# Performance work log

Hardware: AMD Instinct MI355X
Metric: run time of the kernel (lower is better)

## Reference

```python
import jax, jax.numpy as jnp
import numpy as np

FRAC_BITS = 16            # fixed-point fractional bits (MPC fixedpoint precision)
SCALE = float(1 << FRAC_BITS)

def fxp(v):
    """Emulate dup_with_precision: round value to the fixed-point grid with
    FRAC_BITS fractional bits. Straight-through (identity) gradient, matching
    the MPC backward pass which propagates gradients through truncation."""
    return v + jax.lax.stop_gradient(jnp.round(v * SCALE) / SCALE - v)


def setup_inputs() -> dict:
    key = jax.random.key(0)
    kx, kw = jax.random.split(key)
    in_dim, out_dim, batch = 4096, 4096, 2048
    x = jax.random.normal(kx, (batch, in_dim), dtype=jnp.float32)
    # Dense_Local init: w ~ N(0, 1/sqrt(in_dim+1)), b = zeros
    w = jax.random.normal(kw, (in_dim, out_dim), dtype=jnp.float32) / np.sqrt(in_dim + 1)
    b = jnp.zeros((out_dim,), dtype=jnp.float32)
    return {"x": x, "w": w, "b": b}


def reference(x, w, b):
    # quantize operands to the fixed-point grid (values live on the grid in MPC)
    xq = fxp(x)
    wq = fxp(w)
    # y = x @ w, then dup_with_precision(x.fixedpoint): truncate product back
    y = fxp(jnp.matmul(xq, wq))           # [batch, out_dim]
    # + bias
    y = y + fxp(b)
    # secure ReLU: s = drelu_local(y) (sign bit), y = relu(y, s) = y * s
    s = y >= 0
    y = jnp.where(s, y, jnp.zeros((), dtype=y.dtype))
    # final dup_with_precision(new_fixedpoint=x.fixedpoint)
    return fxp(y)
```

## Files before the change

kernel.cpp:

```cpp
#include <hip/hip_runtime.h>
#include <hip/hip_bf16.h>
#include <stdint.h>

#define M_DIM 2048
#define N_DIM 4096
#define K_DIM 4096

#define NT 64

typedef short short8 __attribute__((ext_vector_type(8)));
typedef float f32x4 __attribute__((ext_vector_type(4)));

typedef __attribute__((address_space(1))) unsigned int gu32;
typedef __attribute__((address_space(3))) unsigned int lu32;

__device__ static inline unsigned short f32_to_bf16(float f) {
  union { float f; unsigned int u; } v; v.f = f;
  unsigned int u = v.u;
  u += 0x7FFFu + ((u >> 16) & 1u);
  return (unsigned short)(u >> 16);
}

__global__ void cvt_x_kernel(const float* __restrict__ in, unsigned short* __restrict__ out) {
  size_t i = ((size_t)blockIdx.x * blockDim.x + threadIdx.x) * 8;
  f32x4 a = *(const f32x4*)(in + i);
  f32x4 b = *(const f32x4*)(in + i + 4);
  short8 o;
  o[0] = (short)f32_to_bf16(a[0]); o[1] = (short)f32_to_bf16(a[1]);
  o[2] = (short)f32_to_bf16(a[2]); o[3] = (short)f32_to_bf16(a[3]);
  o[4] = (short)f32_to_bf16(b[0]); o[5] = (short)f32_to_bf16(b[1]);
  o[6] = (short)f32_to_bf16(b[2]); o[7] = (short)f32_to_bf16(b[3]);
  *(short8*)(out + i) = o;
}

__global__ void transpose_cvt_w_kernel(const float* __restrict__ w, unsigned short* __restrict__ wt) {
  __shared__ unsigned short tile[64][64 + 8];
  int bn = blockIdx.x * 64;
  int bk = blockIdx.y * 64;
  int t = threadIdx.x;
  int c4 = (t & 15) * 4;
  int r0 = t >> 4;
#pragma unroll
  for (int p = 0; p < 4; ++p) {
    int r = r0 + p * 16;
    f32x4 v = *(const f32x4*)(w + (size_t)(bk + r) * N_DIM + bn + c4);
    tile[c4 + 0][r] = f32_to_bf16(v[0]);
    tile[c4 + 1][r] = f32_to_bf16(v[1]);
    tile[c4 + 2][r] = f32_to_bf16(v[2]);
    tile[c4 + 3][r] = f32_to_bf16(v[3]);
  }
  __syncthreads();
  int orow = t >> 2;
  int oc = (t & 3) * 16;
  short8 lo, hi;
#pragma unroll
  for (int j = 0; j < 8; ++j) {
    lo[j] = (short)tile[orow][oc + j];
    hi[j] = (short)tile[orow][oc + 8 + j];
  }
  unsigned short* op = wt + (size_t)(bn + orow) * K_DIM + bk + oc;
  *(short8*)(op) = lo;
  *(short8*)(op + 8) = hi;
}


__global__ __launch_bounds__(512) void gemm8_kernel(
    const unsigned short* __restrict__ A, const unsigned short* __restrict__ Bt,
    const float* __restrict__ bias, float* __restrict__ C) {
  __shared__ unsigned short sm16[3 * 24576];
  char* smem = (char*)&sm16[0];

  const int tid = threadIdx.x;
  const int lane = tid & 63;
  const int w = tid >> 6;
  const int wm = w >> 2, wn = w & 3;

  const int id = blockIdx.x;
  const int x = id & 7, j = id >> 3;
  const int by = ((x >> 2) << 3) + (j >> 2);
  const int bx = ((x & 3) << 2) + (j & 3);
  const int r0 = by * 128, c0 = bx * 256;

  const int l8 = lane >> 3, l7 = lane & 7;
  const int chunkE = ((l7 ^ (l8 & 7)) << 3);
  const unsigned short* Ag = A + (size_t)(r0 + w * 16 + l8) * K_DIM + chunkE;
  const unsigned short* Bg = Bt + (size_t)(c0 + w * 32 + l8) * K_DIM + chunkE;
  const int aL0 = w * 2048;
  const int bL0 = 16384 + w * 4096;

#define GL(gp, ldsoff) __builtin_amdgcn_global_load_lds((gu32*)(gp), (lu32*)(smem + (ldsoff)), 16, 0, 0)
#define STAGE_P0(t, sb)                                       \
  do {                                                        \
    GL(Ag + (size_t)(t) * 64, (sb) + aL0);                    \
    GL(Ag + (size_t)(t) * 64 + 8 * (size_t)K_DIM, (sb) + aL0 + 1024); \
    GL(Bg + (size_t)(t) * 64, (sb) + bL0);                    \
  } while (0)
#define STAGE_P1(t, sb)                                       \
  do {                                                        \
    GL(Bg + (size_t)(t) * 64 + 8 * (size_t)K_DIM, (sb) + bL0 + 1024);  \
    GL(Bg + (size_t)(t) * 64 + 16 * (size_t)K_DIM, (sb) + bL0 + 2048); \
    GL(Bg + (size_t)(t) * 64 + 24 * (size_t)K_DIM, (sb) + bL0 + 3072); \
  } while (0)

  const int l15 = lane & 15, hi = lane >> 4;
  const int aR = (wm * 64 + l15) * 64;
  const int bR = 8192 + (wn * 64 + l15) * 64;
  const int slot0 = ((hi ^ l7) << 3);
  const int slot1 = (((4 + hi) ^ l7) << 3);

  f32x4 acc[4][4] = {};

  STAGE_P0(0, 0); STAGE_P1(0, 0);
  STAGE_P0(1, 49152); STAGE_P1(1, 49152);

  int cs = 0;
  for (int t = 0; t < NT; ++t) {
    const int sE = cs * 24576;
    const int stB = (cs == 0 ? 2 : cs - 1) * 49152;
    const bool doStage = (t + 2) < NT;

    if (t < NT - 1) asm volatile("s_waitcnt vmcnt(6)" ::: "memory");
    else            asm volatile("s_waitcnt vmcnt(0)" ::: "memory");
    asm volatile("s_barrier" ::: "memory");

    {
      short8 a[4], b[4];
#pragma unroll
      for (int m = 0; m < 4; ++m) a[m] = *(const short8*)(sm16 + sE + aR + m * 1024 + slot0);
#pragma unroll
      for (int n = 0; n < 4; ++n) b[n] = *(const short8*)(sm16 + sE + bR + n * 1024 + slot0);
      if (doStage) STAGE_P0(t + 2, stB);
      asm volatile("s_barrier" ::: "memory");
      __builtin_amdgcn_s_setprio(1);
#pragma unroll
      for (int m = 0; m < 4; ++m)
#pragma unroll
        for (int n = 0; n < 4; ++n)
          acc[m][n] = __builtin_amdgcn_mfma_f32_16x16x32_bf16(a[m], b[n], acc[m][n], 0, 0, 0);
      __builtin_amdgcn_s_setprio(0);
      asm volatile("s_barrier" ::: "memory");
    }
    {
      short8 a[4], b[4];
#pragma unroll
      for (int m = 0; m < 4; ++m) a[m] = *(const short8*)(sm16 + sE + aR + m * 1024 + slot1);
#pragma unroll
      for (int n = 0; n < 4; ++n) b[n] = *(const short8*)(sm16 + sE + bR + n * 1024 + slot1);
      if (doStage) STAGE_P1(t + 2, stB);
      asm volatile("s_barrier" ::: "memory");
      __builtin_amdgcn_s_setprio(1);
#pragma unroll
      for (int m = 0; m < 4; ++m)
#pragma unroll
        for (int n = 0; n < 4; ++n)
          acc[m][n] = __builtin_amdgcn_mfma_f32_16x16x32_bf16(a[m], b[n], acc[m][n], 0, 0, 0);
      __builtin_amdgcn_s_setprio(0);
      asm volatile("s_barrier" ::: "memory");
    }
    cs = (cs == 2) ? 0 : cs + 1;
  }

  const float S = 65536.0f, IS = 1.0f / 65536.0f;
  const int lr = hi * 4;
#pragma unroll
  for (int n = 0; n < 4; ++n) {
    int gcol = c0 + wn * 64 + n * 16 + l15;
    float bq = rintf(bias[gcol] * S) * IS;
#pragma unroll
    for (int m = 0; m < 4; ++m) {
      int grow = r0 + wm * 64 + m * 16 + lr;
      float* outp = C + (size_t)grow * N_DIM + gcol;
#pragma unroll
      for (int r = 0; r < 4; ++r) {
        float t = rintf(acc[m][n][r] * S) * IS + bq;
        t = t > 0.0f ? t : 0.0f;
        outp[(size_t)r * N_DIM] = t;
      }
    }
  }
#undef GL
#undef STAGE_P0
#undef STAGE_P1
}

__global__ __launch_bounds__(256, 2) void gemm_fb_kernel(
    const float* __restrict__ Xf, const float* __restrict__ Wf,
    const float* __restrict__ bias, float* __restrict__ C) {
  __shared__ unsigned short As[128][64];
  __shared__ unsigned short Bs[128][64];
  int tid = threadIdx.x;
  int lane = tid & 63;
  int wid = tid >> 6;
  int wr = wid >> 1, wc = wid & 1;
  int r0 = blockIdx.y * 128;
  int c0 = blockIdx.x * 128;
  f32x4 acc[4][4] = {};
  for (int kt = 0; kt < K_DIM / 64; ++kt) {
    __syncthreads();
    int ar = tid >> 1;
    int ac = (tid & 1) * 32;
    const float* xp = Xf + (size_t)(r0 + ar) * K_DIM + kt * 64 + ac;
#pragma unroll
    for (int jj = 0; jj < 8; ++jj) {
      f32x4 v = *(const f32x4*)(xp + jj * 4);
      As[ar][ac + jj * 4 + 0] = f32_to_bf16(v[0]);
      As[ar][ac + jj * 4 + 1] = f32_to_bf16(v[1]);
      As[ar][ac + jj * 4 + 2] = f32_to_bf16(v[2]);
      As[ar][ac + jj * 4 + 3] = f32_to_bf16(v[3]);
    }
    int bk_ = tid >> 2;
    int bc = (tid & 3) * 32;
    const float* wp = Wf + (size_t)(kt * 64 + bk_) * N_DIM + c0 + bc;
#pragma unroll
    for (int jj = 0; jj < 8; ++jj) {
      f32x4 v = *(const f32x4*)(wp + jj * 4);
      Bs[bc + jj * 4 + 0][bk_] = f32_to_bf16(v[0]);
      Bs[bc + jj * 4 + 1][bk_] = f32_to_bf16(v[1]);
      Bs[bc + jj * 4 + 2][bk_] = f32_to_bf16(v[2]);
      Bs[bc + jj * 4 + 3][bk_] = f32_to_bf16(v[3]);
    }
    __syncthreads();
#pragma unroll
    for (int ks = 0; ks < 2; ++ks) {
      int co = ks * 32 + (lane >> 4) * 8;
      int rA = wr * 64 + (lane & 15);
      int rB = wc * 64 + (lane & 15);
      short8 a[4], b[4];
#pragma unroll
      for (int m = 0; m < 4; ++m) a[m] = *(const short8*)&As[rA + m * 16][co];
#pragma unroll
      for (int n = 0; n < 4; ++n) b[n] = *(const short8*)&Bs[rB + n * 16][co];
#pragma unroll
      for (int m = 0; m < 4; ++m)
#pragma unroll
        for (int n = 0; n < 4; ++n)
          acc[m][n] = __builtin_amdgcn_mfma_f32_16x16x32_bf16(a[m], b[n], acc[m][n], 0, 0, 0);
    }
  }
  const float S = 65536.0f, IS = 1.0f / 65536.0f;
  int lr = (lane >> 4) * 4;
  int lc = lane & 15;
#pragma unroll
  for (int n = 0; n < 4; ++n) {
    int gcol = c0 + wc * 64 + n * 16 + lc;
    float bq = rintf(bias[gcol] * S) * IS;
#pragma unroll
    for (int m = 0; m < 4; ++m) {
      int grow = r0 + wr * 64 + m * 16 + lr;
      float* outp = C + (size_t)grow * N_DIM + gcol;
#pragma unroll
      for (int r = 0; r < 4; ++r) {
        float t = rintf(acc[m][n][r] * S) * IS + bq;
        t = t > 0.0f ? t : 0.0f;
        outp[(size_t)r * N_DIM] = t;
      }
    }
  }
}

extern "C" void kernel_launch(void* const* d_in, const int* in_sizes, int n_in,
                              void* d_out, int out_size, void* d_ws, size_t ws_size,
                              hipStream_t stream) {
  const float* x = (const float*)d_in[0];
  const float* w = (const float*)d_in[1];
  const float* b = (const float*)d_in[2];
  float* out = (float*)d_out;

  size_t needA = (size_t)M_DIM * K_DIM * sizeof(unsigned short);
  size_t needB = (size_t)K_DIM * N_DIM * sizeof(unsigned short);

  if (ws_size >= needA + needB) {
    unsigned short* Abf = (unsigned short*)d_ws;
    unsigned short* Btbf = (unsigned short*)((char*)d_ws + needA);
    cvt_x_kernel<<<(M_DIM * (size_t)K_DIM / 8 + 255) / 256, 256, 0, stream>>>(x, Abf);
    transpose_cvt_w_kernel<<<dim3(N_DIM / 64, K_DIM / 64), 256, 0, stream>>>(w, Btbf);
    gemm8_kernel<<<256, 512, 0, stream>>>(Abf, Btbf, b, out);
  } else {
    gemm_fb_kernel<<<dim3(N_DIM / 128, M_DIM / 128), 256, 0, stream>>>(x, w, b, out);
  }
}
```

Measured before the change: 94.33 us.

## Merge half-iteration phases into one per-tile step with a single barrier

```diff
diff --git a/kernel.cpp b/kernel.cpp
--- a/kernel.cpp
+++ b/kernel.cpp
@@ -89,14 +89,11 @@
   const int bL0 = 16384 + w * 4096;
 
 #define GL(gp, ldsoff) __builtin_amdgcn_global_load_lds((gu32*)(gp), (lu32*)(smem + (ldsoff)), 16, 0, 0)
-#define STAGE_P0(t, sb)                                       \
-  do {                                                        \
-    GL(Ag + (size_t)(t) * 64, (sb) + aL0);                    \
-    GL(Ag + (size_t)(t) * 64 + 8 * (size_t)K_DIM, (sb) + aL0 + 1024); \
-    GL(Bg + (size_t)(t) * 64, (sb) + bL0);                    \
-  } while (0)
-#define STAGE_P1(t, sb)                                       \
-  do {                                                        \
+#define STAGE_ALL(t, sb)                                               \
+  do {                                                                 \
+    GL(Ag + (size_t)(t) * 64, (sb) + aL0);                             \
+    GL(Ag + (size_t)(t) * 64 + 8 * (size_t)K_DIM, (sb) + aL0 + 1024);  \
+    GL(Bg + (size_t)(t) * 64, (sb) + bL0);                             \
     GL(Bg + (size_t)(t) * 64 + 8 * (size_t)K_DIM, (sb) + bL0 + 1024);  \
     GL(Bg + (size_t)(t) * 64 + 16 * (size_t)K_DIM, (sb) + bL0 + 2048); \
     GL(Bg + (size_t)(t) * 64 + 24 * (size_t)K_DIM, (sb) + bL0 + 3072); \
@@ -110,8 +107,8 @@
 
   f32x4 acc[4][4] = {};
 
-  STAGE_P0(0, 0); STAGE_P1(0, 0);
-  STAGE_P0(1, 49152); STAGE_P1(1, 49152);
+  STAGE_ALL(0, 0);
+  STAGE_ALL(1, 49152);
 
   int cs = 0;
   for (int t = 0; t < NT; ++t) {
@@ -119,44 +116,35 @@
     const int stB = (cs == 0 ? 2 : cs - 1) * 49152;
     const bool doStage = (t + 2) < NT;
 
-    if (t < NT - 1) asm volatile("s_waitcnt vmcnt(6)" ::: "memory");
-    else            asm volatile("s_waitcnt vmcnt(0)" ::: "memory");
+    if (t < NT - 1) asm volatile("s_waitcnt vmcnt(6) lgkmcnt(0)" ::: "memory");
+    else            asm volatile("s_waitcnt vmcnt(0) lgkmcnt(0)" ::: "memory");
+    __builtin_amdgcn_sched_barrier(0);
     asm volatile("s_barrier" ::: "memory");
 
-    {
-      short8 a[4], b[4];
-#pragma unroll
-      for (int m = 0; m < 4; ++m) a[m] = *(const short8*)(sm16 + sE + aR + m * 1024 + slot0);
-#pragma unroll
-      for (int n = 0; n < 4; ++n) b[n] = *(const short8*)(sm16 + sE + bR + n * 1024 + slot0);
-      if (doStage) STAGE_P0(t + 2, stB);
-      asm volatile("s_barrier" ::: "memory");
-      __builtin_amdgcn_s_setprio(1);
-#pragma unroll
-      for (int m = 0; m < 4; ++m)
-#pragma unroll
-        for (int n = 0; n < 4; ++n)
-          acc[m][n] = __builtin_amdgcn_mfma_f32_16x16x32_bf16(a[m], b[n], acc[m][n], 0, 0, 0);
-      __builtin_amdgcn_s_setprio(0);
-      asm volatile("s_barrier" ::: "memory");
-    }
-    {
-      short8 a[4], b[4];
-#pragma unroll
-      for (int m = 0; m < 4; ++m) a[m] = *(const short8*)(sm16 + sE + aR + m * 1024 + slot1);
-#pragma unroll
-      for (int n = 0; n < 4; ++n) b[n] = *(const short8*)(sm16 + sE + bR + n * 1024 + slot1);
-      if (doStage) STAGE_P1(t + 2, stB);
-      asm volatile("s_barrier" ::: "memory");
-      __builtin_amdgcn_s_setprio(1);
-#pragma unroll
-      for (int m = 0; m < 4; ++m)
-#pragma unroll
-        for (int n = 0; n < 4; ++n)
-          acc[m][n] = __builtin_amdgcn_mfma_f32_16x16x32_bf16(a[m], b[n], acc[m][n], 0, 0, 0);
-      __builtin_amdgcn_s_setprio(0);
-      asm volatile("s_barrier" ::: "memory");
-    }
+    short8 a0[4], b0[4], a1[4], b1[4];
+#pragma unroll
+    for (int m = 0; m < 4; ++m) a0[m] = *(const short8*)(sm16 + sE + aR + m * 1024 + slot0);
+#pragma unroll
+    for (int n = 0; n < 4; ++n) b0[n] = *(const short8*)(sm16 + sE + bR + n * 1024 + slot0);
+    if (doStage) STAGE_ALL(t + 2, stB);
+#pragma unroll
+    for (int m = 0; m < 4; ++m) a1[m] = *(const short8*)(sm16 + sE + aR + m * 1024 + slot1);
+#pragma unroll
+    for (int n = 0; n < 4; ++n) b1[n] = *(const short8*)(sm16 + sE + bR + n * 1024 + slot1);
+
+    __builtin_amdgcn_s_setprio(1);
+#pragma unroll
+    for (int m = 0; m < 4; ++m)
+#pragma unroll
+      for (int n = 0; n < 4; ++n)
+        acc[m][n] = __builtin_amdgcn_mfma_f32_16x16x32_bf16(a0[m], b0[n], acc[m][n], 0, 0, 0);
+#pragma unroll
+    for (int m = 0; m < 4; ++m)
+#pragma unroll
+      for (int n = 0; n < 4; ++n)
+        acc[m][n] = __builtin_amdgcn_mfma_f32_16x16x32_bf16(a1[m], b1[n], acc[m][n], 0, 0, 0);
+    __builtin_amdgcn_s_setprio(0);
+
     cs = (cs == 2) ? 0 : cs + 1;
   }
 
@@ -179,8 +167,7 @@
     }
   }
 #undef GL
-#undef STAGE_P0
-#undef STAGE_P1
+#undef STAGE_ALL
 }
 
 __global__ __launch_bounds__(256, 2) void gemm_fb_kernel(
```

Measured after the change: 90.88 us. 3.6% less time.
